# Performance work log

Measured on AMD Instinct MI355X. Metric: run time of the kernel, lower is better.

## Reference

```python
import jax, jax.numpy as jnp
import numpy as np

B, TM1, ENC, DEC, OUT = 256, 32, 128, 128, 1


def setup_inputs() -> dict:
    key = jax.random.key(0)
    ks = jax.random.split(key, 16)
    s = 0.05
    inp = {
        "input_encoded": jax.random.normal(ks[0], (B, TM1, ENC), jnp.float32),
        "y_history": jax.random.normal(ks[1], (B, TM1, OUT), jnp.float32),
        # attn_layer: Linear(2*DEC+ENC -> ENC), Tanh, Linear(ENC -> 1)
        "attn_W1": jax.random.normal(ks[2], (ENC, 2 * DEC + ENC), jnp.float32) * s,
        "attn_b1": jnp.zeros((ENC,), jnp.float32),
        "attn_W2": jax.random.normal(ks[3], (1, ENC), jnp.float32) * s,
        "attn_b2": jnp.zeros((1,), jnp.float32),
        # LSTM(input_size=OUT, hidden_size=DEC), pytorch gate order i,f,g,o
        "W_ih": jax.random.normal(ks[4], (4 * DEC, OUT), jnp.float32) * s,
        "W_hh": jax.random.normal(ks[5], (4 * DEC, DEC), jnp.float32) * s,
        "b_ih": jnp.zeros((4 * DEC,), jnp.float32),
        "b_hh": jnp.zeros((4 * DEC,), jnp.float32),
        # fc: Linear(ENC+OUT -> OUT), weight initialized with normal_() in torch
        "fc_W": jax.random.normal(ks[6], (OUT, ENC + OUT), jnp.float32),
        "fc_b": jnp.zeros((OUT,), jnp.float32),
        # fc_final: Linear(DEC+ENC -> OUT)
        "fcf_W": jax.random.normal(ks[7], (OUT, DEC + ENC), jnp.float32) * s,
        "fcf_b": jnp.zeros((OUT,), jnp.float32),
    }
    return inp


def _forward(input_encoded, y_history, attn_W1, attn_b1, attn_W2, attn_b2,
             W_ih, W_hh, b_ih, b_hh, fc_W, fc_b, fcf_W, fcf_b):
    b, tm1, enc = input_encoded.shape
    dec = W_hh.shape[1]

    h0 = jnp.zeros((b, dec), input_encoded.dtype)
    c0 = jnp.zeros((b, dec), input_encoded.dtype)
    ctx0 = jnp.zeros((b, enc), input_encoded.dtype)

    def step(carry, y_t):  # y_t: [B, OUT]
        h, c, _ = carry
        hc = jnp.concatenate([h, c], axis=-1)  # [B, 2*DEC]
        x = jnp.concatenate(
            [jnp.broadcast_to(hc[:, None, :], (b, tm1, 2 * dec)), input_encoded],
            axis=-1)  # [B, T-1, 2*DEC+ENC]
        hdn = jnp.tanh(jnp.einsum('bte,he->bth', x, attn_W1) + attn_b1)
        logits = jnp.einsum('bth,oh->bto', hdn, attn_W2)[..., 0] + attn_b2[0]  # [B, T-1]
        attn = jax.nn.softmax(logits, axis=1)
        ctx = jnp.einsum('bt,bte->be', attn, input_encoded)  # [B, ENC]
        y_tilde = jnp.concatenate([ctx, y_t], axis=1) @ fc_W.T + fc_b  # [B, OUT]
        gates = y_tilde @ W_ih.T + b_ih + h @ W_hh.T + b_hh  # [B, 4*DEC]
        i, f, g, o = jnp.split(gates, 4, axis=-1)
        c_new = jax.nn.sigmoid(f) * c + jax.nn.sigmoid(i) * jnp.tanh(g)
        h_new = jax.nn.sigmoid(o) * jnp.tanh(c_new)
        return (h_new, c_new, ctx), None

    (h, c, ctx), _ = jax.lax.scan(step, (h0, c0, ctx0),
                                  jnp.swapaxes(y_history, 0, 1))
    out = jnp.concatenate([h, ctx], axis=1) @ fcf_W.T + fcf_b + y_history[:, -1]
    return out  # [B, OUT]


def reference(input_encoded, y_history, attn_W1, attn_b1, attn_W2, attn_b2,
              W_ih, W_hh, b_ih, b_hh, fc_W, fc_b, fcf_W, fcf_b):
    return _forward(input_encoded, y_history, attn_W1, attn_b1, attn_W2, attn_b2,
                    W_ih, W_hh, b_ih, b_hh, fc_W, fc_b, fcf_W, fcf_b)
```

## Files before the change

kernel.cpp:

```cpp
#include <hip/hip_runtime.h>


#define TT 32

typedef _Float16 h2_t __attribute__((ext_vector_type(2)));
typedef _Float16 h4_t __attribute__((ext_vector_type(4)));
typedef _Float16 h8_t __attribute__((ext_vector_type(8)));

#if __has_builtin(__builtin_amdgcn_fdot2)
#define FDOT2(a, b, c) __builtin_amdgcn_fdot2((a), (b), (c), false)
#else
static __device__ __forceinline__ float FDOT2(h2_t a, h2_t b, float c) {
    return c + (float)a[0] * (float)b[0] + (float)a[1] * (float)b[1];
}
#endif

__device__ __forceinline__ float dot_h8(h8_t w, h8_t v, float acc) {
    acc = FDOT2(__builtin_shufflevector(w, w, 0, 1), __builtin_shufflevector(v, v, 0, 1), acc);
    acc = FDOT2(__builtin_shufflevector(w, w, 2, 3), __builtin_shufflevector(v, v, 2, 3), acc);
    acc = FDOT2(__builtin_shufflevector(w, w, 4, 5), __builtin_shufflevector(v, v, 4, 5), acc);
    acc = FDOT2(__builtin_shufflevector(w, w, 6, 7), __builtin_shufflevector(v, v, 6, 7), acc);
    return acc;
}
__device__ __forceinline__ h8_t pk8(float4 a, float4 b) {
    h8_t r;
    r[0] = (_Float16)a.x; r[1] = (_Float16)a.y; r[2] = (_Float16)a.z; r[3] = (_Float16)a.w;
    r[4] = (_Float16)b.x; r[5] = (_Float16)b.y; r[6] = (_Float16)b.z; r[7] = (_Float16)b.w;
    return r;
}
__device__ __forceinline__ float fast_tanh(float x) {
    x = fminf(fmaxf(x, -15.f), 15.f);
    float e = __expf(2.f * x);
    return 1.f - __fdividef(2.f, e + 1.f);
}
__device__ __forceinline__ float fast_sig(float x) {
    return __fdividef(1.f, 1.f + __expf(-x));
}

__global__ __launch_bounds__(1024, 4) void decoder_kernel(
    const float* __restrict__ enc_g,
    const float* __restrict__ yh_g,
    const float* __restrict__ W1,
    const float* __restrict__ b1,
    const float* __restrict__ W2,
    const float* __restrict__ b2,
    const float* __restrict__ Wih,
    const float* __restrict__ Whh,
    const float* __restrict__ bih,
    const float* __restrict__ bhh,
    const float* __restrict__ fcW,
    const float* __restrict__ fcB,
    const float* __restrict__ fcfW,
    const float* __restrict__ fcfB,
    float* __restrict__ out)
{
    __shared__ __align__(16) h8_t s_whh8[512 * 16];
    __shared__ __align__(16) _Float16 s_enc16[TT * 136];
    __shared__ __align__(16) _Float16 s_epre16[TT * 128];
    __shared__ __align__(16) float s_A[128];
    __shared__ __align__(16) float s_w2[128];
    __shared__ __align__(16) float s_gdot[512];
    __shared__ __align__(16) _Float16 s_wih16[512];
    __shared__ __align__(16) _Float16 s_hc16[256];
    __shared__ float s_logit[TT];
    __shared__ float s_q[TT];
    __shared__ float s_att[TT];
    __shared__ float s_yh[TT];
    __shared__ float s_ytilde;

    const int tid = threadIdx.x;
    const int b = blockIdx.x;

    {
        const float4* encp = (const float4*)(enc_g + (size_t)b * TT * 128);
        float4 v = encp[tid];
        int t = tid >> 5, e4 = tid & 31;
        h4_t hv;
        hv[0] = (_Float16)v.x; hv[1] = (_Float16)v.y;
        hv[2] = (_Float16)v.z; hv[3] = (_Float16)v.w;
        *(h4_t*)(s_enc16 + t * 136 + e4 * 4) = hv;
    }
    if (tid < 256) s_hc16[tid] = (_Float16)0.f;
    if (tid < 128) s_w2[tid] = W2[tid];
    if (tid < TT) s_yh[tid] = yh_g[b * TT + tid];

    float bias_r = 0.f;
    h8_t w1a[8];
    if (tid < 512) {
        const int r = tid, rx = r & 15;
        const float4* wp = (const float4*)(Whh + (size_t)r * 128);
#pragma unroll
        for (int c = 0; c < 16; c++)
            s_whh8[(r << 4) | (c ^ rx)] = pk8(wp[2 * c], wp[2 * c + 1]);
        s_wih16[r] = (_Float16)Wih[r];
        bias_r = bih[r] + bhh[r];
    } else {
        const int u = tid - 512, g = u >> 2, s4 = u & 3;
        const float4* p = (const float4*)(W1 + g * 384 + s4 * 64);
#pragma unroll
        for (int k = 0; k < 8; k++) w1a[k] = pk8(p[2 * k], p[2 * k + 1]);
    }
    const float b2v = b2[0];
    const float fcw128 = fcW[128];
    const float fcbv = fcB[0];
    const float fcfbv = fcfB[0];
    __syncthreads();

    {
        const int g8 = tid >> 3, s8 = tid & 7;
        const float4* wp = (const float4*)(W1 + g8 * 384 + 256 + s8 * 16);
        h8_t wa = pk8(wp[0], wp[1]);
        h8_t wb = pk8(wp[2], wp[3]);
        const float b1v = b1[g8];
        for (int t = 0; t < TT; t++) {
            const h8_t* ep8 = (const h8_t*)(s_enc16 + t * 136);
            float pa = dot_h8(wa, ep8[s8 * 2], 0.f);
            pa = dot_h8(wb, ep8[s8 * 2 + 1], pa);
            pa += __shfl_xor(pa, 1);
            pa += __shfl_xor(pa, 2);
            pa += __shfl_xor(pa, 4);
            if (s8 == 0) s_epre16[t * 128 + g8] = (_Float16)(pa + b1v);
        }
    }
    if (tid < 256) {
        const int t = tid >> 3, s8 = tid & 7;
        const float4* fp = (const float4*)(fcW + s8 * 16);
        h8_t fa = pk8(fp[0], fp[1]);
        h8_t fb = pk8(fp[2], fp[3]);
        const h8_t* ep8 = (const h8_t*)(s_enc16 + t * 136);
        float pq = dot_h8(fa, ep8[s8 * 2], 0.f);
        pq = dot_h8(fb, ep8[s8 * 2 + 1], pq);
        pq += __shfl_xor(pq, 1);
        pq += __shfl_xor(pq, 2);
        pq += __shfl_xor(pq, 4);
        if (s8 == 0) s_q[t] = pq;
    }
    __syncthreads();

    const h8_t* hcp8 = (const h8_t*)s_hc16;
    float c_reg = 0.f;

#define GDOT(c, acc) acc = dot_h8(s_whh8[base | ((c) ^ rx)], hcp8[(c)], acc)

    for (int t = 0; t < TT; t++) {
        float pg0 = 0.f, pg1 = 0.f;
        if (tid < 512) {
            const int rx = tid & 15, base = tid << 4;
            GDOT(0, pg0); GDOT(1, pg1); GDOT(2, pg0);
            GDOT(3, pg1); GDOT(4, pg0); GDOT(5, pg1);
        } else {
            const int u = tid - 512, g = u >> 2, s4 = u & 3;
            float a0 = 0.f, a1 = 0.f;
#pragma unroll
            for (int k = 0; k < 8; k += 2) {
                a0 = dot_h8(w1a[k], hcp8[s4 * 8 + k], a0);
                a1 = dot_h8(w1a[k + 1], hcp8[s4 * 8 + k + 1], a1);
            }
            float aa = a0 + a1;
            aa += __shfl_xor(aa, 1);
            aa += __shfl_xor(aa, 2);
            if (s4 == 0) s_A[g] = aa;
        }
        __syncthreads();

        if (tid < 512) {
            const int rx = tid & 15, base = tid << 4;
            GDOT(6, pg0); GDOT(7, pg1); GDOT(8, pg0);
            GDOT(9, pg1); GDOT(10, pg0);
        } else {
            const int u = tid - 512, tt_ = u >> 4, sub = u & 15;
            h8_t ev = *(const h8_t*)(s_epre16 + tt_ * 128 + sub * 8);
            float4 av0 = *(const float4*)(s_A + sub * 8);
            float4 av1 = *(const float4*)(s_A + sub * 8 + 4);
            float4 wv0 = *(const float4*)(s_w2 + sub * 8);
            float4 wv1 = *(const float4*)(s_w2 + sub * 8 + 4);
            float lp = wv0.x * fast_tanh(av0.x + (float)ev[0]) +
                       wv0.y * fast_tanh(av0.y + (float)ev[1]) +
                       wv0.z * fast_tanh(av0.z + (float)ev[2]) +
                       wv0.w * fast_tanh(av0.w + (float)ev[3]) +
                       wv1.x * fast_tanh(av1.x + (float)ev[4]) +
                       wv1.y * fast_tanh(av1.y + (float)ev[5]) +
                       wv1.z * fast_tanh(av1.z + (float)ev[6]) +
                       wv1.w * fast_tanh(av1.w + (float)ev[7]);
            lp += __shfl_xor(lp, 1);
            lp += __shfl_xor(lp, 2);
            lp += __shfl_xor(lp, 4);
            lp += __shfl_xor(lp, 8);
            if (sub == 0) s_logit[tt_] = lp + b2v;
        }
        __syncthreads();

        if (tid < 512) {
            const int rx = tid & 15, base = tid << 4;
            GDOT(11, pg1); GDOT(12, pg0); GDOT(13, pg1);
            GDOT(14, pg0); GDOT(15, pg1);
            s_gdot[tid] = pg0 + pg1 + bias_r;
        } else if (tid < 576) {
            const int lane = tid & 63;
            float el = 0.f, ql = 0.f;
            if (lane < TT) { el = __expf(s_logit[lane]); ql = s_q[lane]; }
            float ss = el, ys = el * ql;
#pragma unroll
            for (int m = 1; m < 64; m <<= 1) {
                ss += __shfl_xor(ss, m);
                ys += __shfl_xor(ys, m);
            }
            float inv = __fdividef(1.f, ss);
            if (lane < TT) s_att[lane] = el * inv;
            if (lane == 0) s_ytilde = ys * inv + fcw128 * s_yh[t] + fcbv;
        }
        __syncthreads();

        if (tid < 128) {
            const float yt = s_ytilde;
            float gi_ = s_gdot[tid] + (float)s_wih16[tid] * yt;
            float gf_ = s_gdot[128 + tid] + (float)s_wih16[128 + tid] * yt;
            float gg_ = s_gdot[256 + tid] + (float)s_wih16[256 + tid] * yt;
            float go_ = s_gdot[384 + tid] + (float)s_wih16[384 + tid] * yt;
            float cn = fast_sig(gf_) * c_reg + fast_sig(gi_) * fast_tanh(gg_);
            float hn = fast_sig(go_) * fast_tanh(cn);
            c_reg = cn;
            s_hc16[tid] = (_Float16)hn;
            s_hc16[128 + tid] = (_Float16)cn;
        }
        __syncthreads();
    }
#undef GDOT

    if (tid >= 512 && tid < 576) {
        const int lane = tid & 63;
        float c0 = 0.f, c1 = 0.f;
        for (int t = 0; t < TT; t++) {
            float a = s_att[t];
            c0 += a * (float)s_enc16[t * 136 + lane];
            c1 += a * (float)s_enc16[t * 136 + 64 + lane];
        }
        float h0 = (float)s_hc16[lane];
        float h1 = (float)s_hc16[64 + lane];
        float p = fcfW[lane] * h0 + fcfW[64 + lane] * h1 +
                  fcfW[128 + lane] * c0 + fcfW[192 + lane] * c1;
#pragma unroll
        for (int m = 1; m < 64; m <<= 1) p += __shfl_xor(p, m);
        if (lane == 0) out[b] = p + fcfbv + s_yh[TT - 1];
    }
}

extern "C" void kernel_launch(void* const* d_in, const int* in_sizes, int n_in,
                              void* d_out, int out_size, void* d_ws, size_t ws_size,
                              hipStream_t stream) {
    decoder_kernel<<<256, 1024, 0, stream>>>(
        (const float*)d_in[0], (const float*)d_in[1], (const float*)d_in[2],
        (const float*)d_in[3], (const float*)d_in[4], (const float*)d_in[5],
        (const float*)d_in[6], (const float*)d_in[7], (const float*)d_in[8],
        (const float*)d_in[9], (const float*)d_in[10], (const float*)d_in[11],
        (const float*)d_in[12], (const float*)d_in[13], (float*)d_out);
}
```

Measured before the change: 172.6 us.

## Merge LSTM update into softmax wave, cut one barrier per step

Folds the LSTM cell update into the single wave that computes the softmax and y_tilde, so each timestep needs three block barriers instead of four. The W_hh dot products are redistributed into two phases of eight chunks. Each of the 64 lanes now updates two hidden units, with W_ih held in registers, and writes h and c into four padded replicas to reduce LDS bank conflicts for the W1 readers. Attention inputs move to fp16 and the tanh clamp is removed, which trades some accuracy and overflow safety for fewer instructions. The final context reduction is spread over 128 threads.

```diff
diff --git a/kernel.cpp b/kernel.cpp
--- a/kernel.cpp
+++ b/kernel.cpp
@@ -29,7 +29,6 @@
     return r;
 }
 __device__ __forceinline__ float fast_tanh(float x) {
-    x = fminf(fmaxf(x, -15.f), 15.f);
     float e = __expf(2.f * x);
     return 1.f - __fdividef(2.f, e + 1.f);
 }
@@ -57,19 +56,20 @@
     __shared__ __align__(16) h8_t s_whh8[512 * 16];
     __shared__ __align__(16) _Float16 s_enc16[TT * 136];
     __shared__ __align__(16) _Float16 s_epre16[TT * 128];
-    __shared__ __align__(16) float s_A[128];
-    __shared__ __align__(16) float s_w2[128];
+    __shared__ __align__(16) _Float16 s_hcx[4 * 272];
+    __shared__ __align__(16) _Float16 s_A16[128];
+    __shared__ __align__(16) _Float16 s_w216[128];
     __shared__ __align__(16) float s_gdot[512];
     __shared__ __align__(16) _Float16 s_wih16[512];
-    __shared__ __align__(16) _Float16 s_hc16[256];
     __shared__ float s_logit[TT];
     __shared__ float s_q[TT];
     __shared__ float s_att[TT];
     __shared__ float s_yh[TT];
-    __shared__ float s_ytilde;
+    __shared__ float s_ctx[128];
 
     const int tid = threadIdx.x;
     const int b = blockIdx.x;
+    const int lane = tid & 63;
 
     {
         const float4* encp = (const float4*)(enc_g + (size_t)b * TT * 128);
@@ -80,8 +80,8 @@
         hv[2] = (_Float16)v.z; hv[3] = (_Float16)v.w;
         *(h4_t*)(s_enc16 + t * 136 + e4 * 4) = hv;
     }
-    if (tid < 256) s_hc16[tid] = (_Float16)0.f;
-    if (tid < 128) s_w2[tid] = W2[tid];
+    if (tid < 544) ((unsigned int*)s_hcx)[tid] = 0u;
+    if (tid < 128) s_w216[tid] = (_Float16)W2[tid];
     if (tid < TT) s_yh[tid] = yh_g[b * TT + tid];
 
     float bias_r = 0.f;
@@ -135,10 +135,15 @@
         pq += __shfl_xor(pq, 4);
         if (s8 == 0) s_q[t] = pq;
     }
+    h8_t w8wih;
+    float c0r = 0.f, c1r = 0.f;
+    if (tid >= 512 && tid < 576) {
+#pragma unroll
+        for (int j = 0; j < 8; j++) w8wih[j] = s_wih16[j * 64 + lane];
+    }
     __syncthreads();
 
-    const h8_t* hcp8 = (const h8_t*)s_hc16;
-    float c_reg = 0.f;
+    const h8_t* hcp8 = (const h8_t*)s_hcx;
 
 #define GDOT(c, acc) acc = dot_h8(s_whh8[base | ((c) ^ rx)], hcp8[(c)], acc)
 
@@ -146,42 +151,38 @@
         float pg0 = 0.f, pg1 = 0.f;
         if (tid < 512) {
             const int rx = tid & 15, base = tid << 4;
-            GDOT(0, pg0); GDOT(1, pg1); GDOT(2, pg0);
-            GDOT(3, pg1); GDOT(4, pg0); GDOT(5, pg1);
+            GDOT(0, pg0); GDOT(1, pg1); GDOT(2, pg0); GDOT(3, pg1);
+            GDOT(4, pg0); GDOT(5, pg1); GDOT(6, pg0); GDOT(7, pg1);
         } else {
             const int u = tid - 512, g = u >> 2, s4 = u & 3;
+            const h8_t* hp = (const h8_t*)(s_hcx + s4 * 272);
             float a0 = 0.f, a1 = 0.f;
 #pragma unroll
             for (int k = 0; k < 8; k += 2) {
-                a0 = dot_h8(w1a[k], hcp8[s4 * 8 + k], a0);
-                a1 = dot_h8(w1a[k + 1], hcp8[s4 * 8 + k + 1], a1);
+                a0 = dot_h8(w1a[k], hp[s4 * 8 + k], a0);
+                a1 = dot_h8(w1a[k + 1], hp[s4 * 8 + k + 1], a1);
             }
             float aa = a0 + a1;
             aa += __shfl_xor(aa, 1);
             aa += __shfl_xor(aa, 2);
-            if (s4 == 0) s_A[g] = aa;
+            if (s4 == 0) s_A16[g] = (_Float16)aa;
         }
         __syncthreads();
 
         if (tid < 512) {
             const int rx = tid & 15, base = tid << 4;
-            GDOT(6, pg0); GDOT(7, pg1); GDOT(8, pg0);
-            GDOT(9, pg1); GDOT(10, pg0);
+            GDOT(8, pg0); GDOT(9, pg1); GDOT(10, pg0); GDOT(11, pg1);
+            GDOT(12, pg0); GDOT(13, pg1); GDOT(14, pg0); GDOT(15, pg1);
+            s_gdot[tid] = pg0 + pg1 + bias_r;
         } else {
             const int u = tid - 512, tt_ = u >> 4, sub = u & 15;
-            h8_t ev = *(const h8_t*)(s_epre16 + tt_ * 128 + sub * 8);
-            float4 av0 = *(const float4*)(s_A + sub * 8);
-            float4 av1 = *(const float4*)(s_A + sub * 8 + 4);
-            float4 wv0 = *(const float4*)(s_w2 + sub * 8);
-            float4 wv1 = *(const float4*)(s_w2 + sub * 8 + 4);
-            float lp = wv0.x * fast_tanh(av0.x + (float)ev[0]) +
-                       wv0.y * fast_tanh(av0.y + (float)ev[1]) +
-                       wv0.z * fast_tanh(av0.z + (float)ev[2]) +
-                       wv0.w * fast_tanh(av0.w + (float)ev[3]) +
-                       wv1.x * fast_tanh(av1.x + (float)ev[4]) +
-                       wv1.y * fast_tanh(av1.y + (float)ev[5]) +
-                       wv1.z * fast_tanh(av1.z + (float)ev[6]) +
-                       wv1.w * fast_tanh(av1.w + (float)ev[7]);
+            h8_t ev = ((const h8_t*)(s_epre16 + tt_ * 128))[sub];
+            h8_t av = ((const h8_t*)s_A16)[sub];
+            h8_t wv = ((const h8_t*)s_w216)[sub];
+            float lp = 0.f;
+#pragma unroll
+            for (int i = 0; i < 8; i++)
+                lp += (float)wv[i] * fast_tanh((float)av[i] + (float)ev[i]);
             lp += __shfl_xor(lp, 1);
             lp += __shfl_xor(lp, 2);
             lp += __shfl_xor(lp, 4);
@@ -190,13 +191,7 @@
         }
         __syncthreads();
 
-        if (tid < 512) {
-            const int rx = tid & 15, base = tid << 4;
-            GDOT(11, pg1); GDOT(12, pg0); GDOT(13, pg1);
-            GDOT(14, pg0); GDOT(15, pg1);
-            s_gdot[tid] = pg0 + pg1 + bias_r;
-        } else if (tid < 576) {
-            const int lane = tid & 63;
+        if (tid >= 512 && tid < 576) {
             float el = 0.f, ql = 0.f;
             if (lane < TT) { el = __expf(s_logit[lane]); ql = s_q[lane]; }
             float ss = el, ys = el * ql;
@@ -207,38 +202,47 @@
             }
             float inv = __fdividef(1.f, ss);
             if (lane < TT) s_att[lane] = el * inv;
-            if (lane == 0) s_ytilde = ys * inv + fcw128 * s_yh[t] + fcbv;
+            float yt = ys * inv + fcw128 * s_yh[t] + fcbv;
+            float g0 = s_gdot[lane]       + (float)w8wih[0] * yt;
+            float g1 = s_gdot[64 + lane]  + (float)w8wih[1] * yt;
+            float g2 = s_gdot[128 + lane] + (float)w8wih[2] * yt;
+            float g3 = s_gdot[192 + lane] + (float)w8wih[3] * yt;
+            float g4 = s_gdot[256 + lane] + (float)w8wih[4] * yt;
+            float g5 = s_gdot[320 + lane] + (float)w8wih[5] * yt;
+            float g6 = s_gdot[384 + lane] + (float)w8wih[6] * yt;
+            float g7 = s_gdot[448 + lane] + (float)w8wih[7] * yt;
+            float cn0 = fast_sig(g2) * c0r + fast_sig(g0) * fast_tanh(g4);
+            float cn1 = fast_sig(g3) * c1r + fast_sig(g1) * fast_tanh(g5);
+            float hn0 = fast_sig(g6) * fast_tanh(cn0);
+            float hn1 = fast_sig(g7) * fast_tanh(cn1);
+            c0r = cn0; c1r = cn1;
+            _Float16 h0 = (_Float16)hn0, h1 = (_Float16)hn1;
+            _Float16 cc0 = (_Float16)cn0, cc1 = (_Float16)cn1;
+#pragma unroll
+            for (int j = 0; j < 4; j++) {
+                _Float16* bp = s_hcx + j * 272;
+                bp[lane] = h0;
+                bp[64 + lane] = h1;
+                bp[128 + lane] = cc0;
+                bp[192 + lane] = cc1;
+            }
         }
         __syncthreads();
-
-        if (tid < 128) {
-            const float yt = s_ytilde;
-            float gi_ = s_gdot[tid] + (float)s_wih16[tid] * yt;
-            float gf_ = s_gdot[128 + tid] + (float)s_wih16[128 + tid] * yt;
-            float gg_ = s_gdot[256 + tid] + (float)s_wih16[256 + tid] * yt;
-            float go_ = s_gdot[384 + tid] + (float)s_wih16[384 + tid] * yt;
-            float cn = fast_sig(gf_) * c_reg + fast_sig(gi_) * fast_tanh(gg_);
-            float hn = fast_sig(go_) * fast_tanh(cn);
-            c_reg = cn;
-            s_hc16[tid] = (_Float16)hn;
-            s_hc16[128 + tid] = (_Float16)cn;
-        }
-        __syncthreads();
     }
 #undef GDOT
 
-    if (tid >= 512 && tid < 576) {
-        const int lane = tid & 63;
-        float c0 = 0.f, c1 = 0.f;
-        for (int t = 0; t < TT; t++) {
-            float a = s_att[t];
-            c0 += a * (float)s_enc16[t * 136 + lane];
-            c1 += a * (float)s_enc16[t * 136 + 64 + lane];
-        }
-        float h0 = (float)s_hc16[lane];
-        float h1 = (float)s_hc16[64 + lane];
-        float p = fcfW[lane] * h0 + fcfW[64 + lane] * h1 +
-                  fcfW[128 + lane] * c0 + fcfW[192 + lane] * c1;
+    if (tid < 128) {
+        float acc = 0.f;
+#pragma unroll 8
+        for (int t = 0; t < TT; t++) acc += s_att[t] * (float)s_enc16[t * 136 + tid];
+        s_ctx[tid] = acc;
+    }
+    __syncthreads();
+    if (tid < 64) {
+        float p = fcfW[lane] * (float)s_hcx[lane] +
+                  fcfW[64 + lane] * (float)s_hcx[64 + lane] +
+                  fcfW[128 + lane] * s_ctx[lane] +
+                  fcfW[192 + lane] * s_ctx[64 + lane];
 #pragma unroll
         for (int m = 1; m < 64; m <<= 1) p += __shfl_xor(p, m);
         if (lane == 0) out[b] = p + fcfbv + s_yh[TT - 1];
```

After: 173.8 us. No clear change (+0.7%).
